# Kernel tuning notes

Hardware: AMD Instinct MI355X
Metric: run time of the kernel (lower is better)

## Reference

```python
import jax, jax.numpy as jnp
import numpy as np

N, G, P, E = 65536, 256, 256, 1048576   # nodes, graphs, nodes/graph, edges
AF, BF, D, H, L, CE, T = 92, 41, 64, 128, 3, 16, 4
EPS = 1e-5


def _lin(x, W, b):
    return x @ W + b


def setup_inputs() -> dict:
    key = jax.random.key(0)
    ks = jax.random.split(key, 32)
    f = jax.random.normal
    inp = {
        "x": f(ks[0], (N, AF), jnp.float32),
        "edge_attr": f(ks[1], (E, BF), jnp.float32),
        "charge": f(ks[2], (G,), jnp.float32),
        "charge_W": f(ks[3], (1, CE)) * 0.3,
        "charge_b": f(ks[4], (CE,)) * 0.1,
        "atom_W": f(ks[5], (AF + CE, D)) * (1.0 / np.sqrt(AF + CE)),
        "atom_b": f(ks[6], (D,)) * 0.1,
        "bond_W": f(ks[7], (BF, D)) * (1.0 / np.sqrt(BF)),
        "bond_b": f(ks[8], (D,)) * 0.1,
        "nu_W1": f(ks[9], (L, 2 * D, D)) * (1.0 / np.sqrt(2 * D)),
        "nu_b1": f(ks[10], (L, D)) * 0.1,
        "nu_W2": f(ks[11], (L, D, D)) * (1.0 / np.sqrt(D)),
        "nu_b2": f(ks[12], (L, D)) * 0.1,
        "eu_W1": f(ks[13], (L, 3 * D, D)) * (1.0 / np.sqrt(3 * D)),
        "eu_b1": f(ks[14], (L, D)) * 0.1,
        "eu_W2": f(ks[15], (L, D, D)) * (1.0 / np.sqrt(D)),
        "eu_b2": f(ks[16], (L, D)) * 0.1,
        "bn_gamma": jnp.ones((L, D), jnp.float32),
        "bn_beta": jnp.zeros((L, D), jnp.float32),
        "pred_W1": f(ks[17], (D, H)) * (1.0 / np.sqrt(D)),
        "pred_b1": f(ks[18], (H,)) * 0.1,
        "pred_W2": f(ks[19], (H, H)) * (1.0 / np.sqrt(H)),
        "pred_b2": f(ks[20], (H,)) * 0.1,
        "pred_W3": f(ks[21], (H, 1)) * (1.0 / np.sqrt(H)),
        "pred_b3": f(ks[22], (1,)) * 0.1,
        "edge_index": jax.random.randint(ks[23], (2, E), 0, N, jnp.int32),
        "batch": (jnp.arange(N, dtype=jnp.int32) // P),
        "target_site_indices": jax.random.randint(ks[24], (G, T), 0, P, jnp.int32),
    }
    return inp


def reference(x, edge_attr, charge, charge_W, charge_b, atom_W, atom_b, bond_W,
              bond_b, nu_W1, nu_b1, nu_W2, nu_b2, eu_W1, eu_b1, eu_W2, eu_b2,
              bn_gamma, bn_beta, pred_W1, pred_b1, pred_W2, pred_b2, pred_W3,
              pred_b3, edge_index, batch, target_site_indices):
    sp = jax.nn.softplus
    # early charge integration
    charge_feat = _lin(charge[:, None], charge_W, charge_b)        # [G, CE]
    h = _lin(jnp.concatenate([x, charge_feat[batch]], 1), atom_W, atom_b)  # [N, D]
    e = _lin(edge_attr, bond_W, bond_b)                            # [E, D]
    row, col = edge_index[0], edge_index[1]
    for i in range(L):
        hs, hd = h[row], h[col]                                    # gather per edge
        e = _lin(sp(_lin(jnp.concatenate([hs, hd, e], 1), eu_W1[i], eu_b1[i])),
                 eu_W2[i], eu_b2[i])                               # edge update
        m = _lin(sp(_lin(jnp.concatenate([hs, e], 1), nu_W1[i], nu_b1[i])),
                 nu_W2[i], nu_b2[i])                               # messages
        hn = jax.ops.segment_sum(m, col, num_segments=N)           # scatter_add
        mu = hn.mean(0)
        var = hn.var(0)                                            # biased, as torch BN train
        hn = (hn - mu) / jnp.sqrt(var + EPS) * bn_gamma[i] + bn_beta[i]
        h = sp(hn) + h
    # selective pooling over target sites (vectorized version of per-graph loop)
    counts = jax.ops.segment_sum(jnp.ones((N,), h.dtype), batch, num_segments=G)
    counts_i = counts.astype(jnp.int32)
    starts = (jnp.cumsum(counts_i) - counts_i)                     # [G] graph offsets
    valid = target_site_indices < counts_i[:, None]                # [G, T]
    gidx = starts[:, None] + jnp.where(valid, target_site_indices, 0)
    sel = h[gidx] * valid[:, :, None].astype(h.dtype)              # [G, T, D]
    nsel = valid.sum(1)
    sel_mean = sel.sum(1) / jnp.maximum(nsel, 1)[:, None].astype(h.dtype)
    gmean = jax.ops.segment_sum(h, batch, num_segments=G) / counts[:, None]
    graph_repr = jnp.where((nsel > 0)[:, None], sel_mean, gmean)   # [G, D]
    # predictor (dropout = identity in eval)
    z = sp(_lin(graph_repr, pred_W1, pred_b1))
    z = sp(_lin(z, pred_W2, pred_b2))
    out = _lin(z, pred_W3, pred_b3)
    return out.squeeze(-1)                                         # [G]
```

## Files before the change

### kernel.cpp

```cpp
#include <hip/hip_runtime.h>
#include <hip/hip_bf16.h>
#include <hip/hip_fp16.h>
#include <math.h>

#define N_NODES 65536
#define N_GRAPH 256
#define P_NODES 256
#define N_EDGES 1048576
#define AF 92
#define BF 41
#define DIM 64
#define HID 128
#define NLAYER 3
#define CE 16
#define TS 4
#define BN_EPS 1e-5f
#define EPW 32
#define PSTRIDE 33

typedef _Float16 half8 __attribute__((ext_vector_type(8)));
typedef float floatx4 __attribute__((ext_vector_type(4)));

__device__ __forceinline__ float softplus_f(float x) {
    return fmaxf(x, 0.0f) + __logf(1.0f + __expf(-fabsf(x)));
}

__global__ __launch_bounds__(64) void k_h0(
    const float* __restrict__ x, const float* __restrict__ charge,
    const float* __restrict__ chW, const float* __restrict__ chb,
    const float* __restrict__ atomW, const float* __restrict__ atomb,
    const int* __restrict__ batch, float* __restrict__ h)
{
    const int n = blockIdx.x * 64 + threadIdx.x;
    float acc[DIM];
#pragma unroll
    for (int j = 0; j < DIM; ++j) acc[j] = atomb[j];
    const float* xr = x + (size_t)n * AF;
    for (int k2 = 0; k2 < AF; k2 += 2) {
        float2 a = *(const float2*)(xr + k2);
        {
            const float* w = atomW + (size_t)k2 * DIM;
#pragma unroll
            for (int j = 0; j < DIM; ++j) acc[j] = fmaf(w[j], a.x, acc[j]);
        }
        {
            const float* w = atomW + (size_t)(k2 + 1) * DIM;
#pragma unroll
            for (int j = 0; j < DIM; ++j) acc[j] = fmaf(w[j], a.y, acc[j]);
        }
    }
    const float cg = charge[batch[n]];
#pragma unroll
    for (int k = 0; k < CE; ++k) {
        float av = fmaf(cg, chW[k], chb[k]);
        const float* w = atomW + (size_t)(AF + k) * DIM;
#pragma unroll
        for (int j = 0; j < DIM; ++j) acc[j] = fmaf(w[j], av, acc[j]);
    }
    float* hp = h + (size_t)n * DIM;
#pragma unroll
    for (int j = 0; j < DIM; j += 4)
        *(float4*)(hp + j) = make_float4(acc[j], acc[j+1], acc[j+2], acc[j+3]);
}

__global__ __launch_bounds__(128) void k_e0(
    const float* __restrict__ eattr, const float* __restrict__ bondW,
    const float* __restrict__ bondb, const int* __restrict__ ipos,
    __half* __restrict__ eT)
{
    const int t = blockIdx.x * 128 + threadIdx.x;
    float acc[DIM];
#pragma unroll
    for (int j = 0; j < DIM; ++j) acc[j] = bondb[j];
    const float* ar = eattr + (size_t)t * BF;
    for (int k = 0; k < BF; ++k) {
        float av = ar[k];
        const float* w = bondW + (size_t)k * DIM;
#pragma unroll
        for (int j = 0; j < DIM; ++j) acc[j] = fmaf(w[j], av, acc[j]);
    }
    const int slot = ipos[t];
    _Float16* epp = (_Float16*)(eT + (size_t)slot * DIM);
#pragma unroll
    for (int j = 0; j < DIM; j += 8) {
        half8 hv;
#pragma unroll
        for (int u = 0; u < 8; ++u) hv[u] = (_Float16)acc[j + u];
        *(half8*)(epp + j) = hv;
    }
}

__global__ __launch_bounds__(256) void k_hist(const int* __restrict__ ecol,
                                              int* __restrict__ cnt)
{
    int t = blockIdx.x * 256 + threadIdx.x;
    atomicAdd(&cnt[ecol[t]], 1);
}

__global__ __launch_bounds__(256) void k_scan(const int* __restrict__ cnt,
                                              int* __restrict__ starts)
{
    __shared__ int ps[256];
    const int t = threadIdx.x;
    int s = 0;
    for (int i = 0; i < 256; ++i) s += cnt[t * 256 + i];
    ps[t] = s;
    __syncthreads();
    for (int off = 1; off < 256; off <<= 1) {
        int v = (t >= off) ? ps[t - off] : 0;
        __syncthreads();
        ps[t] += v;
        __syncthreads();
    }
    int run = ps[t] - s;
    for (int i = 0; i < 256; ++i) {
        starts[t * 256 + i] = run;
        run += cnt[t * 256 + i];
    }
    if (t == 255) starts[N_NODES] = run;
}

__global__ __launch_bounds__(256) void k_scatter(const int* __restrict__ ecol,
                                                 int* __restrict__ cur,
                                                 int* __restrict__ perm,
                                                 int* __restrict__ ipos)
{
    int t = blockIdx.x * 256 + threadIdx.x;
    int pos = atomicAdd(&cur[ecol[t]], 1);
    perm[pos] = t;
    ipos[t] = pos;
}

__global__ __launch_bounds__(256) void k_wprep_all(
    const float* __restrict__ euW1, const float* __restrict__ euW2,
    const float* __restrict__ nuW1, const float* __restrict__ nuW2,
    __half* __restrict__ out)
{
    const int idx = blockIdx.x * 256 + threadIdx.x;
    const int layer = idx / 28672;
    int off = idx - layer * 28672;
    const float* W;
    if (off < 12288)        { W = euW1 + (size_t)layer * 192 * DIM; }
    else if (off < 16384)   { W = euW2 + (size_t)layer * DIM * DIM; off -= 12288; }
    else if (off < 24576)   { W = nuW1 + (size_t)layer * 128 * DIM; off -= 16384; }
    else                    { W = nuW2 + (size_t)layer * DIM * DIM; off -= 24576; }
    int j    = off & 7;
    int lane = (off >> 3) & 63;
    int f    = off >> 9;
    int ntile = f & 3;
    int kIter = f >> 2;
    int k = kIter * 32 + ((lane >> 4) & 3) * 8 + j;
    int n = ntile * 16 + (lane & 15);
    out[idx] = __float2half(W[k * 64 + n]);
}

__device__ __forceinline__ void init_acc(floatx4 acc[2][4],
                                         const float* __restrict__ b, int mrow)
{
#pragma unroll
    for (int n = 0; n < 4; ++n) {
        float bv = b[n * 16 + mrow];
        floatx4 f = {bv, bv, bv, bv};
        acc[0][n] = f;
        acc[1][n] = f;
    }
}

__device__ __forceinline__ void gemm_panel(floatx4 acc[2][4],
                                           const _Float16* __restrict__ P,
                                           const __half* __restrict__ Wf,
                                           int fragBase, int quad,
                                           int mrow, int lane)
{
    const _Float16* Wh = (const _Float16*)Wf;
#pragma unroll
    for (int ki = 0; ki < 2; ++ki) {
        const _Float16* pa = P + (size_t)(((ki * 4 + quad) * PSTRIDE + mrow) * 8);
        half8 a0 = *(const half8*)pa;
        half8 a1 = *(const half8*)(pa + 16 * 8);
#pragma unroll
        for (int n = 0; n < 4; ++n) {
            half8 b = *(const half8*)(Wh +
                ((size_t)(fragBase + ki * 4 + n) * 64 + lane) * 8);
            acc[0][n] = __builtin_amdgcn_mfma_f32_16x16x32_f16(a0, b, acc[0][n], 0, 0, 0);
            acc[1][n] = __builtin_amdgcn_mfma_f32_16x16x32_f16(a1, b, acc[1][n], 0, 0, 0);
        }
    }
}

__device__ __forceinline__ void cstore_panel(const floatx4 acc[2][4],
                                             _Float16* __restrict__ P,
                                             int quad, int mrow, bool sp)
{
#pragma unroll
    for (int t = 0; t < 2; ++t)
#pragma unroll
        for (int n = 0; n < 4; ++n)
#pragma unroll
            for (int r = 0; r < 4; ++r) {
                int edge = t * 16 + quad * 4 + r;
                int d = n * 16 + mrow;
                float v = acc[t][n][r];
                if (sp) v = softplus_f(v);
                P[((d >> 3) * PSTRIDE + edge) * 8 + (d & 7)] = (_Float16)v;
            }
}

__device__ __forceinline__ void rows_to_global(const _Float16* __restrict__ P,
                                               __half* __restrict__ dst,
                                               int e0, int lane)
{
#pragma unroll
    for (int i = 0; i < 4; ++i) {
        int idx = i * 64 + lane;
        int eL = idx >> 3;
        int c  = idx & 7;
        half8 v = *(const half8*)&P[(c * PSTRIDE + eL) * 8];
        *(half8*)((_Float16*)dst + (size_t)(e0 + eL) * 64 + c * 8) = v;
    }
}

__device__ __forceinline__ void stage_h(const float* __restrict__ hrow,
                                        _Float16* __restrict__ P,
                                        int sEdge, int sSeg)
{
    const float* hp = hrow + sSeg * 32;
#pragma unroll
    for (int i = 0; i < 4; ++i) {
        float4 v0 = *(const float4*)(hp + i * 8);
        float4 v1 = *(const float4*)(hp + i * 8 + 4);
        half8 hv;
        hv[0] = (_Float16)v0.x; hv[1] = (_Float16)v0.y;
        hv[2] = (_Float16)v0.z; hv[3] = (_Float16)v0.w;
        hv[4] = (_Float16)v1.x; hv[5] = (_Float16)v1.y;
        hv[6] = (_Float16)v1.z; hv[7] = (_Float16)v1.w;
        *(half8*)&P[((sSeg * 4 + i) * PSTRIDE + sEdge) * 8] = hv;
    }
}

__global__ __launch_bounds__(64) void k_edge4(
    const float* __restrict__ h, __half* __restrict__ eT,
    const __half* __restrict__ Wf,
    const float* __restrict__ eub1, const float* __restrict__ eub2,
    const float* __restrict__ nub1, const float* __restrict__ nub2,
    const int* __restrict__ erow, const int* __restrict__ ecol,
    const int* __restrict__ perm,
    __half* __restrict__ m)
{
    __shared__ __align__(16) _Float16 P0[8 * PSTRIDE * 8];
    __shared__ __align__(16) _Float16 P1[8 * PSTRIDE * 8];
    const int lane = threadIdx.x;
    const int quad = lane >> 4;
    const int mrow = lane & 15;
    const int e0   = blockIdx.x * EPW;
    const int sEdge = lane >> 1;
    const int sSeg  = lane & 1;

    floatx4 acc[2][4];

    half8 epre[4];
    {
        const _Float16* ep = (const _Float16*)(eT + (size_t)(e0 + sEdge) * DIM) + sSeg * 32;
#pragma unroll
        for (int i = 0; i < 4; ++i) epre[i] = *(const half8*)(ep + i * 8);
    }

    const int ed = perm[e0 + sEdge];
    stage_h(h + (size_t)erow[ed] * DIM, P0, sEdge, sSeg);
    stage_h(h + (size_t)ecol[ed] * DIM, P1, sEdge, sSeg);
    __syncthreads();

    init_acc(acc, eub1, mrow);
    gemm_panel(acc, P0, Wf, 0, quad, mrow, lane);
    gemm_panel(acc, P1, Wf, 8, quad, mrow, lane);
    __syncthreads();
    {
#pragma unroll
        for (int i = 0; i < 4; ++i)
            *(half8*)&P1[((sSeg * 4 + i) * PSTRIDE + sEdge) * 8] = epre[i];
    }
    __syncthreads();
    gemm_panel(acc, P1, Wf, 16, quad, mrow, lane);
    __syncthreads();
    cstore_panel(acc, P1, quad, mrow, true);
    __syncthreads();

    init_acc(acc, eub2, mrow);
    gemm_panel(acc, P1, Wf, 24, quad, mrow, lane);
    __syncthreads();
    cstore_panel(acc, P1, quad, mrow, false);
    __syncthreads();
    rows_to_global(P1, eT, e0, lane);

    init_acc(acc, nub1, mrow);
    gemm_panel(acc, P0, Wf, 32, quad, mrow, lane);
    gemm_panel(acc, P1, Wf, 40, quad, mrow, lane);
    __syncthreads();
    cstore_panel(acc, P0, quad, mrow, true);
    __syncthreads();

    init_acc(acc, nub2, mrow);
    gemm_panel(acc, P0, Wf, 48, quad, mrow, lane);
    __syncthreads();
    cstore_panel(acc, P1, quad, mrow, false);
    __syncthreads();
    rows_to_global(P1, m, e0, lane);
}

__global__ __launch_bounds__(256) void k_agg(
    const __half2* __restrict__ m2, const int* __restrict__ starts,
    float* __restrict__ hn)
{
    const int w = threadIdx.x >> 6;
    const int lane = threadIdx.x & 63;
    const int n = blockIdx.x * 4 + w;
    const int s = starts[n], e = starts[n + 1];
    const int r = lane >> 5, d2 = lane & 31;
    float ax = 0.f, ay = 0.f;
    for (int i = s + r; i < e; i += 2) {
        float2 f = __half22float2(m2[(size_t)i * 32 + d2]);
        ax += f.x; ay += f.y;
    }
    ax += __shfl(ax, lane ^ 32, 64);
    ay += __shfl(ay, lane ^ 32, 64);
    if (r == 0) *(float2*)(hn + (size_t)n * DIM + d2 * 2) = make_float2(ax, ay);
}

__global__ __launch_bounds__(256) void k_bnstats(const float* __restrict__ hn,
                                                 float* __restrict__ stats)
{
    const int j = threadIdx.x & 63;
    const int sub = threadIdx.x >> 6;
    const int r0 = blockIdx.x * 256;
    float s = 0.f, qq = 0.f;
    for (int i = 0; i < 64; ++i) {
        float v = hn[(size_t)(r0 + i * 4 + sub) * DIM + j];
        s += v;
        qq = fmaf(v, v, qq);
    }
    __shared__ float ls[256], lq[256];
    ls[threadIdx.x] = s; lq[threadIdx.x] = qq;
    __syncthreads();
    if (threadIdx.x < 128) {
        ls[threadIdx.x] += ls[threadIdx.x + 128];
        lq[threadIdx.x] += lq[threadIdx.x + 128];
    }
    __syncthreads();
    if (threadIdx.x < 64) {
        atomicAdd(&stats[j],      ls[threadIdx.x] + ls[threadIdx.x + 64]);
        atomicAdd(&stats[64 + j], lq[threadIdx.x] + lq[threadIdx.x + 64]);
    }
}

__global__ __launch_bounds__(256) void k_hupd(
    const float* __restrict__ hn, float* __restrict__ h,
    const float* __restrict__ stats, const float* __restrict__ gamma,
    const float* __restrict__ beta)
{
    const size_t idx = (size_t)blockIdx.x * 256 + threadIdx.x;
    const int j = (int)(idx & 63);
    const float inv_n = 1.0f / (float)N_NODES;
    float mu  = stats[j] * inv_n;
    float var = stats[64 + j] * inv_n - mu * mu;
    float sc  = gamma[j] * rsqrtf(var + BN_EPS);
    float v   = (hn[idx] - mu) * sc + beta[j];
    h[idx] += softplus_f(v);
}

__global__ __launch_bounds__(64) void k_pool(const float* __restrict__ h,
                                             const int* __restrict__ tsi,
                                             float* __restrict__ gr)
{
    const int g = blockIdx.x, j = threadIdx.x;
    float s = 0.f;
#pragma unroll
    for (int t = 0; t < TS; ++t) {
        int p = tsi[g * TS + t];
        s += h[(size_t)(g * P_NODES + p) * DIM + j];
    }
    gr[g * DIM + j] = s * (1.0f / TS);
}

__global__ __launch_bounds__(128) void k_pred(const float* __restrict__ gr,
    const float* __restrict__ W1, const float* __restrict__ b1,
    const float* __restrict__ W2, const float* __restrict__ b2,
    const float* __restrict__ W3, const float* __restrict__ b3,
    float* __restrict__ out)
{
    const int g = blockIdx.x, j = threadIdx.x;
    __shared__ float zin[DIM], z1[HID], red[HID];
    if (j < DIM) zin[j] = gr[g * DIM + j];
    __syncthreads();
    float a = b1[j];
    for (int k = 0; k < DIM; ++k) a = fmaf(zin[k], W1[k * HID + j], a);
    z1[j] = softplus_f(a);
    __syncthreads();
    float a2 = b2[j];
    for (int k = 0; k < HID; ++k) a2 = fmaf(z1[k], W2[k * HID + j], a2);
    red[j] = softplus_f(a2) * W3[j];
    __syncthreads();
    for (int s = 64; s > 0; s >>= 1) {
        if (j < s) red[j] += red[j + s];
        __syncthreads();
    }
    if (j == 0) out[g] = red[0] + b3[0];
}

extern "C" void kernel_launch(void* const* d_in, const int* in_sizes, int n_in,
                              void* d_out, int out_size, void* d_ws, size_t ws_size,
                              hipStream_t stream)
{
    const float* x      = (const float*)d_in[0];
    const float* eattr  = (const float*)d_in[1];
    const float* charge = (const float*)d_in[2];
    const float* chW    = (const float*)d_in[3];
    const float* chb    = (const float*)d_in[4];
    const float* atomW  = (const float*)d_in[5];
    const float* atomb  = (const float*)d_in[6];
    const float* bondW  = (const float*)d_in[7];
    const float* bondb  = (const float*)d_in[8];
    const float* nuW1   = (const float*)d_in[9];
    const float* nub1   = (const float*)d_in[10];
    const float* nuW2   = (const float*)d_in[11];
    const float* nub2   = (const float*)d_in[12];
    const float* euW1   = (const float*)d_in[13];
    const float* eub1   = (const float*)d_in[14];
    const float* euW2   = (const float*)d_in[15];
    const float* eub2   = (const float*)d_in[16];
    const float* gamma  = (const float*)d_in[17];
    const float* beta   = (const float*)d_in[18];
    const float* pW1    = (const float*)d_in[19];
    const float* pb1    = (const float*)d_in[20];
    const float* pW2    = (const float*)d_in[21];
    const float* pb2    = (const float*)d_in[22];
    const float* pW3    = (const float*)d_in[23];
    const float* pb3    = (const float*)d_in[24];
    const int*   eidx   = (const int*)d_in[25];
    const int*   batch  = (const int*)d_in[26];
    const int*   tsi    = (const int*)d_in[27];
    const int* erow = eidx;
    const int* ecol = eidx + N_EDGES;

    char* ws = (char*)d_ws;
    float*  h      = (float*)(ws);
    float*  hn     = (float*)(ws + ((size_t)16 << 20));
    int*    ipos   = (int*)  (ws + ((size_t)16 << 20));
    float*  stats  = (float*)(ws + ((size_t)32 << 20));
    float*  gr     = (float*)(ws + ((size_t)32 << 20) + (64 << 10));
    int*    counts = (int*)  (ws + ((size_t)33 << 20));
    int*    starts = (int*)  (ws + ((size_t)33 << 20) + (256 << 10));
    int*    cur    = (int*)  (ws + ((size_t)33 << 20) + (768 << 10));
    __half* Wfrag  = (__half*)(ws + ((size_t)34 << 20));
    int*    perm   = (int*)  (ws + ((size_t)35 << 20));
    __half* eT     = (__half*)(ws + ((size_t)40 << 20));
    __half* m      = (__half*)(ws + ((size_t)168 << 20));

    hipMemsetAsync(counts, 0, N_NODES * sizeof(int), stream);
    k_hist<<<N_EDGES / 256, 256, 0, stream>>>(ecol, counts);
    k_scan<<<1, 256, 0, stream>>>(counts, starts);
    hipMemcpyAsync(cur, starts, N_NODES * sizeof(int),
                   hipMemcpyDeviceToDevice, stream);
    k_scatter<<<N_EDGES / 256, 256, 0, stream>>>(ecol, cur, perm, ipos);

    k_wprep_all<<<(3 * 28672) / 256, 256, 0, stream>>>(euW1, euW2, nuW1, nuW2, Wfrag);

    k_h0<<<N_NODES / 64, 64, 0, stream>>>(x, charge, chW, chb, atomW, atomb, batch, h);
    k_e0<<<N_EDGES / 128, 128, 0, stream>>>(eattr, bondW, bondb, ipos, eT);

    const size_t LW = 28672;
    for (int i = 0; i < NLAYER; ++i) {
        hipMemsetAsync(stats, 0, 128 * sizeof(float), stream);
        k_edge4<<<N_EDGES / EPW, 64, 0, stream>>>(h, eT, Wfrag + i * LW,
            eub1 + i * DIM, eub2 + i * DIM, nub1 + i * DIM, nub2 + i * DIM,
            erow, ecol, perm, m);
        k_agg<<<N_NODES / 4, 256, 0, stream>>>((const __half2*)m, starts, hn);
        k_bnstats<<<N_NODES / 256, 256, 0, stream>>>(hn, stats);
        k_hupd<<<(N_NODES * DIM) / 256, 256, 0, stream>>>(hn, h, stats,
            gamma + i * DIM, beta + i * DIM);
    }

    k_pool<<<N_GRAPH, 64, 0, stream>>>(h, tsi, gr);
    k_pred<<<N_GRAPH, HID, 0, stream>>>(gr, pW1, pb1, pW2, pb2, pW3, pb3, (float*)d_out);
}
```

Before: 1.502 ms.

## Compute bond embedding with MFMA fp16 tiles and coalesced edge staging

```diff
diff --git a/kernel.cpp b/kernel.cpp
--- a/kernel.cpp
+++ b/kernel.cpp
@@ -61,33 +61,6 @@
 #pragma unroll
     for (int j = 0; j < DIM; j += 4)
         *(float4*)(hp + j) = make_float4(acc[j], acc[j+1], acc[j+2], acc[j+3]);
-}
-
-__global__ __launch_bounds__(128) void k_e0(
-    const float* __restrict__ eattr, const float* __restrict__ bondW,
-    const float* __restrict__ bondb, const int* __restrict__ ipos,
-    __half* __restrict__ eT)
-{
-    const int t = blockIdx.x * 128 + threadIdx.x;
-    float acc[DIM];
-#pragma unroll
-    for (int j = 0; j < DIM; ++j) acc[j] = bondb[j];
-    const float* ar = eattr + (size_t)t * BF;
-    for (int k = 0; k < BF; ++k) {
-        float av = ar[k];
-        const float* w = bondW + (size_t)k * DIM;
-#pragma unroll
-        for (int j = 0; j < DIM; ++j) acc[j] = fmaf(w[j], av, acc[j]);
-    }
-    const int slot = ipos[t];
-    _Float16* epp = (_Float16*)(eT + (size_t)slot * DIM);
-#pragma unroll
-    for (int j = 0; j < DIM; j += 8) {
-        half8 hv;
-#pragma unroll
-        for (int u = 0; u < 8; ++u) hv[u] = (_Float16)acc[j + u];
-        *(half8*)(epp + j) = hv;
-    }
 }
 
 __global__ __launch_bounds__(256) void k_hist(const int* __restrict__ ecol,
@@ -154,6 +127,20 @@
     out[idx] = __float2half(W[k * 64 + n]);
 }
 
+__global__ __launch_bounds__(256) void k_wprep_bond(
+    const float* __restrict__ bondW, __half* __restrict__ out)
+{
+    const int idx = blockIdx.x * 256 + threadIdx.x;
+    int j    = idx & 7;
+    int lane = (idx >> 3) & 63;
+    int f    = idx >> 9;
+    int ntile = f & 3;
+    int kIter = f >> 2;
+    int k = kIter * 32 + ((lane >> 4) & 3) * 8 + j;
+    int n = ntile * 16 + (lane & 15);
+    out[idx] = (k < BF) ? __float2half(bondW[k * 64 + n]) : __float2half(0.0f);
+}
+
 __device__ __forceinline__ void init_acc(floatx4 acc[2][4],
                                          const float* __restrict__ b, int mrow)
 {
@@ -235,6 +222,72 @@
         hv[4] = (_Float16)v1.x; hv[5] = (_Float16)v1.y;
         hv[6] = (_Float16)v1.z; hv[7] = (_Float16)v1.w;
         *(half8*)&P[((sSeg * 4 + i) * PSTRIDE + sEdge) * 8] = hv;
+    }
+}
+
+__device__ __forceinline__ void stage_e2(_Float16* __restrict__ P,
+                                         int id2, float2 v)
+{
+    int idx = id2 * 2;
+    int e = (idx * 51151) >> 21;
+    int k = idx - e * 41;
+    P[((k >> 3) * PSTRIDE + e) * 8 + (k & 7)] = (_Float16)v.x;
+    idx++;
+    e = (idx * 51151) >> 21;
+    k = idx - e * 41;
+    P[((k >> 3) * PSTRIDE + e) * 8 + (k & 7)] = (_Float16)v.y;
+}
+
+__global__ __launch_bounds__(64) void k_e0m(
+    const float* __restrict__ eattr, const __half* __restrict__ Wb,
+    const float* __restrict__ bondb, const int* __restrict__ ipos,
+    __half* __restrict__ eT)
+{
+    __shared__ __align__(16) _Float16 P0[8 * PSTRIDE * 8];
+    __shared__ int slot[32];
+    const int lane = threadIdx.x;
+    const int quad = lane >> 4;
+    const int mrow = lane & 15;
+    const int e0   = blockIdx.x * 32;
+
+    if (lane < 32) slot[lane] = ipos[e0 + lane];
+
+    {
+        half8 z = {};
+#pragma unroll
+        for (int i = 0; i < 4; ++i) ((half8*)P0)[i * 64 + lane] = z;
+        if (lane < 8) ((half8*)P0)[256 + lane] = z;
+    }
+    __syncthreads();
+
+    const float* src = eattr + (size_t)e0 * BF;
+#pragma unroll
+    for (int i = 0; i < 10; ++i) {
+        const int id2 = i * 64 + lane;
+        float2 v = *(const float2*)(src + id2 * 2);
+        stage_e2(P0, id2, v);
+    }
+    if (lane < 16) {
+        const int id2 = 640 + lane;
+        float2 v = *(const float2*)(src + id2 * 2);
+        stage_e2(P0, id2, v);
+    }
+    __syncthreads();
+
+    floatx4 acc[2][4];
+    init_acc(acc, bondb, mrow);
+    gemm_panel(acc, P0, Wb, 0, quad, mrow, lane);
+    __syncthreads();
+    cstore_panel(acc, P0, quad, mrow, false);
+    __syncthreads();
+
+#pragma unroll
+    for (int i = 0; i < 4; ++i) {
+        int idx = i * 64 + lane;
+        int eL = idx >> 3;
+        int c  = idx & 7;
+        half8 v = *(const half8*)&P0[(c * PSTRIDE + eL) * 8];
+        *(half8*)((_Float16*)eT + (size_t)slot[eL] * DIM + c * 8) = v;
     }
 }
 
@@ -451,6 +504,7 @@
     int*    starts = (int*)  (ws + ((size_t)33 << 20) + (256 << 10));
     int*    cur    = (int*)  (ws + ((size_t)33 << 20) + (768 << 10));
     __half* Wfrag  = (__half*)(ws + ((size_t)34 << 20));
+    __half* Wbond  = (__half*)(ws + ((size_t)34 << 20) + (256 << 10));
     int*    perm   = (int*)  (ws + ((size_t)35 << 20));
     __half* eT     = (__half*)(ws + ((size_t)40 << 20));
     __half* m      = (__half*)(ws + ((size_t)168 << 20));
@@ -463,9 +517,10 @@
     k_scatter<<<N_EDGES / 256, 256, 0, stream>>>(ecol, cur, perm, ipos);
 
     k_wprep_all<<<(3 * 28672) / 256, 256, 0, stream>>>(euW1, euW2, nuW1, nuW2, Wfrag);
+    k_wprep_bond<<<16, 256, 0, stream>>>(bondW, Wbond);
 
     k_h0<<<N_NODES / 64, 64, 0, stream>>>(x, charge, chW, chb, atomW, atomb, batch, h);
-    k_e0<<<N_EDGES / 128, 128, 0, stream>>>(eattr, bondW, bondb, ipos, eT);
+    k_e0m<<<N_EDGES / 32, 64, 0, stream>>>(eattr, Wbond, bondb, ipos, eT);
 
     const size_t LW = 28672;
     for (int i = 0; i < NLAYER; ++i) {
```

Result: faster. 1.327 ms (-11.6%).
